# Performance work log

Measured on AMD Instinct MI355X. Metric: run time of the kernel, lower is better.

Reference implementation:

```python
import math
import jax, jax.numpy as jnp
import numpy as np

B, S, M, D, H = 4, 1024, 8, 64, 8
NF = D // 2  # n_freq = head_dim // 2
BANDWIDTH = 1.0


def setup_inputs() -> dict:
    key = jax.random.key(0)
    ks = jax.random.split(key, 12)
    n = lambda k, shp, sc=1.0: (jax.random.normal(k, shp, dtype=jnp.float32) * sc)
    w_scale = 0.02  # typical init scale for linear weights
    return {
        'q_atoms': n(ks[0], (B, S, M, D)),
        'q_logw': n(ks[1], (B, S, M)),
        'k_atoms': n(ks[2], (B, S, M, D)),
        'k_logw': n(ks[3], (B, S, M)),
        'v_atoms': n(ks[4], (B, S, M, D)),
        'v_logw': n(ks[5], (B, S, M)),
        'Wq': n(ks[6], (H * D, D), w_scale),   # torch Linear weight [out, in]
        'Wk': n(ks[7], (H * D, D), w_scale),
        'Wv': n(ks[8], (H * D, D), w_scale),
        'Wo': n(ks[9], (D, H * D), w_scale),
        'Ww': n(ks[10], (M, D), w_scale * 0.1),  # w_proj.weight scaled by 0.1
        'freqs': n(ks[11], (H, D, NF), 1.0 / BANDWIDTH),  # buffer
    }


def reference(q_atoms, q_logw, k_atoms, k_logw, v_atoms, v_logw,
              Wq, Wk, Wv, Wo, Ww, freqs):
    rff_scale = 1.0 / math.sqrt(NF)
    attn_scale = 1.0 / math.sqrt(D)

    q_w = jax.nn.softmax(q_logw, axis=-1)  # [B,S,M]
    k_w = jax.nn.softmax(k_logw, axis=-1)

    def proj(x, W):  # x: [B,S,M,D], W: [H*D, D] -> [B,S,M,H,D]
        return jnp.einsum('bsmd,ed->bsme', x, W).reshape(B, -1, M, H, D)

    qa = proj(q_atoms, Wq)
    ka = proj(k_atoms, Wk)
    va = proj(v_atoms, Wv)  # [B,S,M,H,D]

    def rff_encode(atoms, weights):
        # atoms: [B,S,M,H,D], weights: [B,S,M] -> [B,H,S,F] with F=D
        p = jnp.einsum('bsmhd,hdf->bsmhf', atoms, freqs)
        phi = jnp.concatenate([jnp.cos(p), jnp.sin(p)], axis=-1) * rff_scale
        z = jnp.einsum('bsmhf,bsm->bshf', phi, weights)
        return z.transpose(0, 2, 1, 3)

    q_enc = rff_encode(qa, q_w)  # [B,H,S,D]
    k_enc = rff_encode(ka, k_w)

    attn = jax.nn.softmax(
        jnp.einsum('bhqf,bhkf->bhqk', q_enc, k_enc) * attn_scale, axis=-1)

    # attn @ values, keeping atom dim m: [B,S,M,H,D]
    out = jnp.einsum('bhqk,bkmhd->bqmhd', attn, va)
    out = out.reshape(B, S, M, H * D)
    out_atoms = out @ Wo.T                  # [B,S,M,D]
    out_features = out_atoms.mean(axis=2)   # [B,S,D]
    new_log_weights = q_logw + out_features @ Ww.T  # [B,S,M]
    return out_atoms, new_log_weights
```

## Files before the change

### kernel.cpp

```cpp
#include <hip/hip_runtime.h>
#include <hip/hip_bf16.h>

typedef __hip_bfloat16 bf16;
typedef __attribute__((ext_vector_type(8))) short short8;
typedef __attribute__((ext_vector_type(4))) float floatx4;

#define CB 4
#define CS 1024
#define CM 8
#define CD 64
#define CH 8
#define CNF 32
#define CHD 512

#define OB_STRIDE 520
#define OS_STRIDE 68
#define AT_STRIDE 72
#define VO_STRIDE 40

__device__ __forceinline__ float b2f(bf16 x) { return __bfloat162float(x); }
__device__ __forceinline__ float us2f(unsigned short u) {
    union { unsigned int i; float f; } v; v.i = ((unsigned int)u) << 16; return v.f;
}
__device__ __forceinline__ floatx4 mfma16(short8 a, short8 b, floatx4 c) {
    return __builtin_amdgcn_mfma_f32_16x16x32_bf16(a, b, c, 0, 0, 0);
}


__global__ __launch_bounds__(256) void prep(const float* __restrict__ Wq,
                                            const float* __restrict__ Wk,
                                            const float* __restrict__ freqs,
                                            const float* __restrict__ Wo,
                                            const float* __restrict__ Wv,
                                            bf16* __restrict__ Fqb,
                                            bf16* __restrict__ Fkb,
                                            bf16* __restrict__ Wof,
                                            bf16* __restrict__ Wvf) {
    int bx = blockIdx.x, t = threadIdx.x;
    if (bx < 128) {
        int which = bx >> 6, h = (bx >> 3) & 7, ec = bx & 7;
        const float* W = which ? Wk : Wq;
        bf16* Fb = which ? Fkb : Fqb;
        int f = t & 31, el = t >> 5;
        int e = ec * 8 + el;
        float acc = 0.f;
        for (int d = 0; d < 64; ++d)
            acc += W[(h * 64 + d) * 64 + e] * freqs[(h * 64 + d) * 32 + f];
        int ntile = h * 2 + (f >> 4);
        int half = e >> 5, quad = (e >> 3) & 3, j = e & 7;
        Fb[(ntile * 2 + half) * 512 + quad * 128 + (f & 15) * 8 + j] = __float2bfloat16(acc);
    } else if (bx < 144) {
        int gid = (bx - 128) * 256 + t;
        #pragma unroll
        for (int i = 0; i < 2; ++i) {
            int idx4 = gid * 2 + i;
            float4 v = ((const float4*)Wo)[idx4];
            int flat = idx4 * 4;
            int o = flat >> 9, k0 = flat & 511;
            int ot = o >> 4, r0 = o & 15;
            int ks = k0 >> 5, qd = (k0 >> 3) & 3, j0 = k0 & 7;
            union { bf16 ob[4]; uint2 u; } pk;
            pk.ob[0] = __float2bfloat16(v.x); pk.ob[1] = __float2bfloat16(v.y);
            pk.ob[2] = __float2bfloat16(v.z); pk.ob[3] = __float2bfloat16(v.w);
            *(uint2*)(Wof + (ot * 16 + ks) * 512 + qd * 128 + r0 * 8 + j0) = pk.u;
        }
    } else {
        int gid = (bx - 144) * 256 + t;
        #pragma unroll
        for (int i = 0; i < 2; ++i) {
            int idx4 = gid * 2 + i;
            float4 v = ((const float4*)Wv)[idx4];
            int flat = idx4 * 4;
            int c = flat >> 6, e0 = flat & 63;
            int h2 = c >> 6, d = c & 63;
            int ehalf = e0 >> 5, qd = (e0 >> 3) & 3, j0 = e0 & 7;
            union { bf16 ob[4]; uint2 u; } pk;
            pk.ob[0] = __float2bfloat16(v.x); pk.ob[1] = __float2bfloat16(v.y);
            pk.ob[2] = __float2bfloat16(v.z); pk.ob[3] = __float2bfloat16(v.w);
            *(uint2*)(Wvf + (h2 * 8 + (d >> 4) * 2 + ehalf) * 512
                          + qd * 128 + (d & 15) * 8 + j0) = pk.u;
        }
    }
}

__global__ __launch_bounds__(256) void encvp(const float* __restrict__ qa_in,
                                             const float* __restrict__ ql,
                                             const float* __restrict__ ka_in,
                                             const float* __restrict__ kl,
                                             const bf16* __restrict__ Fqb,
                                             const bf16* __restrict__ Fkb,
                                             bf16* __restrict__ qf,
                                             bf16* __restrict__ kf,
                                             const float* __restrict__ va_in,
                                             const bf16* __restrict__ Wvf,
                                             bf16* __restrict__ Vt) {
    __shared__ __align__(16) bf16 smem[20480];
    int t = threadIdx.x;
    int w = t >> 6, l = t & 63;
    int quad = l >> 4, r = l & 15;

    if (blockIdx.x < 1024) {
        int blk = blockIdx.x;
        int xbase = blk * 4;
        int b = xbase >> 10, s0 = xbase & 1023;
        float* wgtF = (float*)smem;
        bf16* atq = smem + 128;
        bf16* atk = smem + 128 + 2304;
        bf16* zL  = smem + 128 + 4608;
        int tw = w & 1, nb = (w >> 1) * 8;

        {
            const float* srcq = qa_in + (size_t)(blk * 32) * 64;
            const float* srck = ka_in + (size_t)(blk * 32) * 64;
            #pragma unroll
            for (int j = 0; j < 2; ++j) {
                int idx4 = j * 256 + t;
                int flat = idx4 * 4;
                int row = flat >> 6, e = flat & 63;
                float4 vq = ((const float4*)srcq)[idx4];
                float4 vk = ((const float4*)srck)[idx4];
                union { bf16 ob[4]; uint2 u; } pq, pk2;
                pq.ob[0] = __float2bfloat16(vq.x); pq.ob[1] = __float2bfloat16(vq.y);
                pq.ob[2] = __float2bfloat16(vq.z); pq.ob[3] = __float2bfloat16(vq.w);
                pk2.ob[0] = __float2bfloat16(vk.x); pk2.ob[1] = __float2bfloat16(vk.y);
                pk2.ob[2] = __float2bfloat16(vk.z); pk2.ob[3] = __float2bfloat16(vk.w);
                *(uint2*)(atq + row * AT_STRIDE + e) = pq.u;
                *(uint2*)(atk + row * AT_STRIDE + e) = pk2.u;
            }
        }
        if (t < 64) {
            int which = t >> 5, row = t & 31;
            int si = row >> 3, m = row & 7;
            const float* lwp = (which ? kl : ql) + (size_t)(xbase + si) * 8;
            float lw[8]; float mx = -1e30f;
            #pragma unroll
            for (int j = 0; j < 8; ++j) { lw[j] = lwp[j]; mx = fmaxf(mx, lw[j]); }
            float sm = 0.f;
            #pragma unroll
            for (int j = 0; j < 8; ++j) sm += __expf(lw[j] - mx);
            const float rs = 0.17677669529663687f;
            float osc = which ? rs : rs * 0.125f;
            wgtF[which * 32 + row] = __expf(lw[m] - mx) * (osc / sm);
        }
        __syncthreads();

        for (int which = 0; which < 2; ++which) {
            const bf16* atb2 = which ? atk : atq;
            const bf16* Fb = which ? Fkb : Fqb;

            short8 a0 = *(const short8*)(atb2 + (tw * 16 + r) * AT_STRIDE + quad * 8);
            short8 a1 = *(const short8*)(atb2 + (tw * 16 + r) * AT_STRIDE + quad * 8 + 32);

            floatx4 acc[8];
            #pragma unroll
            for (int nt = 0; nt < 8; ++nt) {
                int ntile = nb + nt;
                short8 b0 = *(const short8*)(Fb + (ntile * 2 + 0) * 512 + l * 8);
                short8 b1 = *(const short8*)(Fb + (ntile * 2 + 1) * 512 + l * 8);
                floatx4 c = {0.f, 0.f, 0.f, 0.f};
                c = mfma16(a0, b0, c);
                c = mfma16(a1, b1, c);
                acc[nt] = c;
            }

            float wv[4];
            #pragma unroll
            for (int reg = 0; reg < 4; ++reg)
                wv[reg] = wgtF[which * 32 + tw * 16 + quad * 4 + reg];

            int si = tw * 2 + (quad >> 1);
            int iss = quad & 1;
            #pragma unroll
            for (int nt = 0; nt < 8; ++nt) {
                int n = (nb + nt) * 16 + r;
                int h = n >> 5, f = n & 31;
                float zc = 0.f, zs = 0.f;
                #pragma unroll
                for (int reg = 0; reg < 4; ++reg) {
                    float sv, cv;
                    __sincosf(acc[nt][reg], &sv, &cv);
                    zc += wv[reg] * cv;
                    zs += wv[reg] * sv;
                }
                zc += __shfl_xor(zc, 16);
                zs += __shfl_xor(zs, 16);
                float val = iss ? zs : zc;
                zL[((which * 4 + si) * 8 + h) * 64 + f + 32 * iss] = __float2bfloat16(val);
            }
        }
        __syncthreads();

        #pragma unroll
        for (int rep = 0; rep < 2; ++rep) {
            int idx = rep * 256 + t;
            int row = idx >> 3, c = idx & 7;
            int which = row >> 5, si = (row >> 3) & 3, h = row & 7;
            bf16* enc = which ? kf : qf;
            short8 v = *(const short8*)(zL + row * 64 + c * 8);
            int s = s0 + si;
            int bh = b * 8 + h;
            int kt = s >> 4, half = c >> 2, qd = c & 3;
            *(short8*)(enc + ((size_t)((bh * 64 + kt) * 2 + half)) * 512
                           + (qd * 16 + (s & 15)) * 8) = v;
        }
    } else {
        int vp = blockIdx.x - 1024;
        int g = vp & 127, h = vp >> 7;
        int b = g >> 5, sc = g & 31;
        int bh = b * 8 + h;
        bf16* atb = smem;
        bf16* os = smem;

        const float* src = va_in + ((size_t)(b * 1024 + sc * 32)) * 512;
        #pragma unroll
        for (int j = 0; j < 16; ++j) {
            int idx4 = j * 256 + t;
            float4 v = ((const float4*)src)[idx4];
            int flat = idx4 * 4;
            int s = flat >> 9, m = (flat >> 6) & 7, e = flat & 63;
            union { bf16 ob[4]; uint2 u; } pk;
            pk.ob[0] = __float2bfloat16(v.x); pk.ob[1] = __float2bfloat16(v.y);
            pk.ob[2] = __float2bfloat16(v.z); pk.ob[3] = __float2bfloat16(v.w);
            *(uint2*)(atb + (m * 32 + s) * AT_STRIDE + e) = pk.u;
        }
        __syncthreads();

        int dhalf = w & 1, sg = w >> 1;
        short8 aw0[2], aw1[2];
        #pragma unroll
        for (int dt = 0; dt < 2; ++dt) {
            int dt4 = dhalf * 2 + dt;
            aw0[dt] = *(const short8*)(Wvf + (size_t)(h * 8 + dt4 * 2 + 0) * 512 + l * 8);
            aw1[dt] = *(const short8*)(Wvf + (size_t)(h * 8 + dt4 * 2 + 1) * 512 + l * 8);
        }
        floatx4 acc[8][2];
        #pragma unroll
        for (int m = 0; m < 8; ++m)
            #pragma unroll
            for (int dt = 0; dt < 2; ++dt) acc[m][dt] = (floatx4){0.f, 0.f, 0.f, 0.f};

        #pragma unroll
        for (int m = 0; m < 8; ++m) {
            short8 b0 = *(const short8*)(atb + (m * 32 + sg * 16 + r) * AT_STRIDE + quad * 8);
            short8 b1 = *(const short8*)(atb + (m * 32 + sg * 16 + r) * AT_STRIDE + quad * 8 + 32);
            #pragma unroll
            for (int dt = 0; dt < 2; ++dt) {
                acc[m][dt] = mfma16(aw0[dt], b0, acc[m][dt]);
                acc[m][dt] = mfma16(aw1[dt], b1, acc[m][dt]);
            }
        }
        __syncthreads();

        #pragma unroll
        for (int m = 0; m < 8; ++m)
            #pragma unroll
            for (int dt = 0; dt < 2; ++dt)
                #pragma unroll
                for (int reg = 0; reg < 4; ++reg) {
                    int n = m * 64 + dhalf * 32 + dt * 16 + quad * 4 + reg;
                    os[n * VO_STRIDE + sg * 16 + r] = __float2bfloat16(acc[m][dt][reg]);
                }
        __syncthreads();

        #pragma unroll
        for (int j = 0; j < 8; ++j) {
            int ch = j * 256 + t;
            int nblk = ch >> 6, lv = ch & 63;
            int rv = lv & 15, qv = lv >> 4;
            short8 v = *(const short8*)(os + (nblk * 16 + rv) * VO_STRIDE + qv * 8);
            *(short8*)(Vt + ((size_t)(bh * 32 + nblk) * 32 + sc) * 512 + lv * 8) = v;
        }
    }
}

__global__ __launch_bounds__(512, 4) void attn_kern(const bf16* __restrict__ qf,
                                                    const bf16* __restrict__ kf,
                                                    const bf16* __restrict__ Vt,
                                                    bf16* __restrict__ tmpf) {
    int n = blockIdx.x;
    int bh = (n & 7) + 8 * (n >> 8);
    int qb = (n >> 3) & 31;
    int b = bh >> 3, h = bh & 7;

    __shared__ __align__(16) bf16 Sc[32 * 1024];
    __shared__ float sumW[8 * 32];
    __shared__ float invL[32];
    int t = threadIdx.x;
    int w = t >> 6, l = t & 63;
    int quad = l >> 4, r = l & 15;
    int k7 = r & 7;

    const bf16* qfb = qf + (size_t)(bh * 128 + qb * 4) * 512 + l * 8;
    short8 q0 = *(const short8*)(qfb);
    short8 q1 = *(const short8*)(qfb + 512);
    short8 q2 = *(const short8*)(qfb + 1024);
    short8 q3 = *(const short8*)(qfb + 1536);

    const bf16* kfb = kf + (size_t)(bh * 128) * 512 + l * 8;
    short8 kr[4][2];
    #pragma unroll
    for (int d = 0; d < 4; ++d) {
        kr[d][0] = *(const short8*)(kfb + (size_t)(w * 8 + d) * 1024);
        kr[d][1] = *(const short8*)(kfb + (size_t)(w * 8 + d) * 1024 + 512);
    }

    float ps0 = 0.f, ps1 = 0.f;
    #pragma unroll
    for (int i = 0; i < 8; ++i) {
        short8 k0 = kr[i & 3][0], k1 = kr[i & 3][1];
        if (i + 4 < 8) {
            kr[i & 3][0] = *(const short8*)(kfb + (size_t)(w * 8 + i + 4) * 1024);
            kr[i & 3][1] = *(const short8*)(kfb + (size_t)(w * 8 + i + 4) * 1024 + 512);
        }
        floatx4 c0 = {0.f, 0.f, 0.f, 0.f}, c1 = {0.f, 0.f, 0.f, 0.f};
        c0 = mfma16(k0, q0, c0); c0 = mfma16(k1, q1, c0);
        c1 = mfma16(k0, q2, c1); c1 = mfma16(k1, q3, c1);
        int ktl = w * 8 + i;
        int chunk = ktl * 2 + (quad >> 1);
        int sw = ((chunk ^ k7) << 3) + (quad & 1) * 4;
        union { uint2 u; bf16 bb[4]; } p0, p1;
        #pragma unroll
        for (int reg = 0; reg < 4; ++reg) {
            float e0 = __expf(c0[reg]);
            float e1 = __expf(c1[reg]);
            ps0 += e0; ps1 += e1;
            p0.bb[reg] = __float2bfloat16(e0);
            p1.bb[reg] = __float2bfloat16(e1);
        }
        *(uint2*)(Sc + r * 1024 + sw) = p0.u;
        *(uint2*)(Sc + (r + 16) * 1024 + sw) = p1.u;
    }
    ps0 += __shfl_xor(ps0, 16); ps0 += __shfl_xor(ps0, 32);
    ps1 += __shfl_xor(ps1, 16); ps1 += __shfl_xor(ps1, 32);
    if (l < 16) {
        sumW[w * 32 + r] = ps0;
        sumW[w * 32 + 16 + r] = ps1;
    }
    __syncthreads();

    if (t < 32) {
        float s = 0.f;
        #pragma unroll
        for (int w2 = 0; w2 < 8; ++w2) s += sumW[w2 * 32 + t];
        invL[t] = 1.f / s;
    }

    floatx4 acc0[4], acc1[4];
    #pragma unroll
    for (int nt = 0; nt < 4; ++nt) {
        acc0[nt] = (floatx4){0.f, 0.f, 0.f, 0.f};
        acc1[nt] = (floatx4){0.f, 0.f, 0.f, 0.f};
    }
    const bf16* vbase = Vt + ((size_t)(bh * 32 + w * 4) * 32) * 512 + l * 8;
    short8 vr[4][4];
    #pragma unroll
    for (int d = 0; d < 4; ++d)
        #pragma unroll
        for (int nt = 0; nt < 4; ++nt)
            vr[d][nt] = *(const short8*)(vbase + nt * 16384 + d * 512);

    #pragma unroll
    for (int ks = 0; ks < 32; ++ks) {
        int pc = (((ks * 4 + quad) ^ k7) << 3);
        short8 pa0 = *(const short8*)(Sc + r * 1024 + pc);
        short8 pa1 = *(const short8*)(Sc + (16 + r) * 1024 + pc);
        __builtin_amdgcn_s_setprio(1);
        #pragma unroll
        for (int nt = 0; nt < 4; ++nt) {
            acc0[nt] = mfma16(pa0, vr[ks & 3][nt], acc0[nt]);
            acc1[nt] = mfma16(pa1, vr[ks & 3][nt], acc1[nt]);
        }
        __builtin_amdgcn_s_setprio(0);
        if (ks + 4 < 32) {
            #pragma unroll
            for (int nt = 0; nt < 4; ++nt)
                vr[ks & 3][nt] = *(const short8*)(vbase + nt * 16384 + (ks + 4) * 512);
        }
    }
    __syncthreads();

    float inv0[4], inv1[4];
    #pragma unroll
    for (int reg = 0; reg < 4; ++reg) {
        inv0[reg] = invL[quad * 4 + reg];
        inv1[reg] = invL[16 + quad * 4 + reg];
    }

    bf16* Ob = Sc;
    #pragma unroll
    for (int nt = 0; nt < 4; ++nt)
        #pragma unroll
        for (int reg = 0; reg < 4; ++reg) {
            int col = w * 64 + nt * 16 + r;
            int m = col >> 6, d = col & 63;
            int colS = m * 64 + ((d + m * 8) & 63);
            Ob[(quad * 4 + reg) * OB_STRIDE + colS] =
                __float2bfloat16(acc0[nt][reg] * inv0[reg]);
            Ob[(quad * 4 + reg + 16) * OB_STRIDE + colS] =
                __float2bfloat16(acc1[nt][reg] * inv1[reg]);
        }
    __syncthreads();

    #pragma unroll
    for (int i = 0; i < 4; ++i) {
        int ci = i * 8 + w;
        int lv = t & 63;
        int T = ci >> 1, khalf = ci & 1;
        int quadv = lv >> 4, rv = lv & 15;
        int p = rv >> 3, m = rv & 7;
        int q_local = T * 2 + p;
        int d0 = khalf * 32 + quadv * 8;
        int colS = m * 64 + ((d0 + m * 8) & 63);
        short8 v = *(const short8*)(Ob + q_local * OB_STRIDE + colS);
        int GT = b * 512 + qb * 16 + T;
        *(short8*)(tmpf + ((size_t)(GT * 16 + h * 2 + khalf)) * 512 + lv * 8) = v;
    }
}

__global__ __launch_bounds__(256) void finalize(const bf16* __restrict__ tmpf,
                                                const bf16* __restrict__ Wof,
                                                const float* __restrict__ Ww,
                                                const float* __restrict__ ql,
                                                float* __restrict__ out) {
    __shared__ __align__(16) float Os[64][OS_STRIDE];
    __shared__ float fs[8][64];
    int t = threadIdx.x;
    int w = t >> 6, l = t & 63;
    int quad = l >> 4, r = l & 15;
    size_t rowbase = (size_t)blockIdx.x * 64;

    floatx4 acc[4];
    #pragma unroll
    for (int nt = 0; nt < 4; ++nt) acc[nt] = (floatx4){0.f, 0.f, 0.f, 0.f};

    const bf16* afrag = tmpf + ((size_t)(blockIdx.x * 4 + w) * 16) * 512 + l * 8;
    const bf16* bfrag = Wof + l * 8;

    for (int ks = 0; ks < 16; ++ks) {
        short8 a = *(const short8*)(afrag + ks * 512);
        #pragma unroll
        for (int nt = 0; nt < 4; ++nt) {
            short8 bb = *(const short8*)(bfrag + (size_t)(nt * 16 + ks) * 512);
            acc[nt] = mfma16(a, bb, acc[nt]);
        }
    }
    #pragma unroll
    for (int nt = 0; nt < 4; ++nt)
        #pragma unroll
        for (int reg = 0; reg < 4; ++reg)
            Os[w * 16 + quad * 4 + reg][nt * 16 + r] = acc[nt][reg];
    __syncthreads();

    #pragma unroll
    for (int i = 0; i < 4; ++i) {
        int ch = i * 256 + t;
        int rr = ch >> 4, c4 = (ch & 15) * 4;
        float4 v = *(const float4*)&Os[rr][c4];
        *(float4*)(out + (rowbase + rr) * 64 + c4) = v;
    }

    {
        int g = t >> 5, oo = (t & 31) * 2;
        float f0 = 0.f, f1 = 0.f;
        #pragma unroll
        for (int m = 0; m < 8; ++m) {
            f0 += Os[g * 8 + m][oo];
            f1 += Os[g * 8 + m][oo + 1];
        }
        fs[g][oo] = f0 * 0.125f;
        fs[g][oo + 1] = f1 * 0.125f;
    }
    __syncthreads();

    if (t < 64) {
        int g = t >> 3, mm = t & 7;
        size_t x = (size_t)blockIdx.x * 8 + g;
        float nl = ql[x * 8 + mm];
        #pragma unroll
        for (int o = 0; o < 64; ++o) nl += fs[g][o] * Ww[mm * 64 + o];
        out[(size_t)CB * CS * CM * CD + x * 8 + mm] = nl;
    }
}

extern "C" void kernel_launch(void* const* d_in, const int* in_sizes, int n_in,
                              void* d_out, int out_size, void* d_ws, size_t ws_size,
                              hipStream_t stream) {
    const float* q_atoms = (const float*)d_in[0];
    const float* q_logw  = (const float*)d_in[1];
    const float* k_atoms = (const float*)d_in[2];
    const float* k_logw  = (const float*)d_in[3];
    const float* v_atoms = (const float*)d_in[4];
    const float* Wq = (const float*)d_in[6];
    const float* Wk = (const float*)d_in[7];
    const float* Wv = (const float*)d_in[8];
    const float* Wo = (const float*)d_in[9];
    const float* Ww = (const float*)d_in[10];
    const float* freqs = (const float*)d_in[11];

    bf16* Fqb = (bf16*)d_ws;
    bf16* Fkb = Fqb + 16384;
    bf16* qf = Fkb + 16384;
    bf16* kf = qf + 2097152;
    bf16* Vt = kf + 2097152;
    bf16* tmpf = Vt + 2097152 * 8;
    bf16* Wof = tmpf + 16777216;
    bf16* Wvf = Wof + 32768;
    float* out = (float*)d_out;

    prep<<<160, 256, 0, stream>>>(Wq, Wk, freqs, Wo, Wv, Fqb, Fkb, Wof, Wvf);
    encvp<<<2048, 256, 0, stream>>>(q_atoms, q_logw, k_atoms, k_logw,
                                    Fqb, Fkb, qf, kf,
                                    v_atoms, Wvf, Vt);
    attn_kern<<<1024, 512, 0, stream>>>(qf, kf, Vt, tmpf);
    finalize<<<CB * CS / 8, 256, 0, stream>>>(tmpf, Wof, Ww, q_logw, out);
}
```

Measured before the change: 172.6 us.

## Fold Wv projection into output weight, attend over raw value atoms

The value projection Wv is no longer applied per token. Instead, Wo and Wv are pre-multiplied per head into a combined weight Cf inside the prep kernel. The attention kernel now reads raw bf16 value atoms, which are shared across all heads, rather than per-head projected values. This removes the per-head V projection GEMM and shrinks the value workspace written by encvp. The cost is an extra small weight-product computation in prep and a strided, uncoalesced scalar transpose of the value atoms.

Result: faster. 167.5 us (-2.9%).

```diff
diff --git a/kernel.cpp b/kernel.cpp
--- a/kernel.cpp
+++ b/kernel.cpp
@@ -16,7 +16,6 @@
 #define OB_STRIDE 520
 #define OS_STRIDE 68
 #define AT_STRIDE 72
-#define VO_STRIDE 40
 
 __device__ __forceinline__ float b2f(bf16 x) { return __bfloat162float(x); }
 __device__ __forceinline__ float us2f(unsigned short u) {
@@ -34,8 +33,7 @@
                                             const float* __restrict__ Wv,
                                             bf16* __restrict__ Fqb,
                                             bf16* __restrict__ Fkb,
-                                            bf16* __restrict__ Wof,
-                                            bf16* __restrict__ Wvf) {
+                                            bf16* __restrict__ Cf) {
     int bx = blockIdx.x, t = threadIdx.x;
     if (bx < 128) {
         int which = bx >> 6, h = (bx >> 3) & 7, ec = bx & 7;
@@ -49,37 +47,25 @@
         int ntile = h * 2 + (f >> 4);
         int half = e >> 5, quad = (e >> 3) & 3, j = e & 7;
         Fb[(ntile * 2 + half) * 512 + quad * 128 + (f & 15) * 8 + j] = __float2bfloat16(acc);
-    } else if (bx < 144) {
-        int gid = (bx - 128) * 256 + t;
-        #pragma unroll
-        for (int i = 0; i < 2; ++i) {
-            int idx4 = gid * 2 + i;
-            float4 v = ((const float4*)Wo)[idx4];
-            int flat = idx4 * 4;
-            int o = flat >> 9, k0 = flat & 511;
-            int ot = o >> 4, r0 = o & 15;
-            int ks = k0 >> 5, qd = (k0 >> 3) & 3, j0 = k0 & 7;
-            union { bf16 ob[4]; uint2 u; } pk;
-            pk.ob[0] = __float2bfloat16(v.x); pk.ob[1] = __float2bfloat16(v.y);
-            pk.ob[2] = __float2bfloat16(v.z); pk.ob[3] = __float2bfloat16(v.w);
-            *(uint2*)(Wof + (ot * 16 + ks) * 512 + qd * 128 + r0 * 8 + j0) = pk.u;
-        }
     } else {
-        int gid = (bx - 144) * 256 + t;
-        #pragma unroll
-        for (int i = 0; i < 2; ++i) {
-            int idx4 = gid * 2 + i;
-            float4 v = ((const float4*)Wv)[idx4];
-            int flat = idx4 * 4;
-            int c = flat >> 6, e0 = flat & 63;
-            int h2 = c >> 6, d = c & 63;
-            int ehalf = e0 >> 5, qd = (e0 >> 3) & 3, j0 = e0 & 7;
-            union { bf16 ob[4]; uint2 u; } pk;
-            pk.ob[0] = __float2bfloat16(v.x); pk.ob[1] = __float2bfloat16(v.y);
-            pk.ob[2] = __float2bfloat16(v.z); pk.ob[3] = __float2bfloat16(v.w);
-            *(uint2*)(Wvf + (h2 * 8 + (d >> 4) * 2 + ehalf) * 512
-                          + qd * 128 + (d & 15) * 8 + j0) = pk.u;
-        }
+        int fid = ((bx - 128) * 256 + t) * 8;
+        int o = fid >> 9, rem = fid & 511, h = rem >> 6, e0 = rem & 63;
+        const float* wo = Wo + o * 512 + h * 64;
+        float accv[8];
+        #pragma unroll
+        for (int i = 0; i < 8; ++i) accv[i] = 0.f;
+        for (int d = 0; d < 64; ++d) {
+            float wod = wo[d];
+            const float* wv = Wv + (size_t)(h * 64 + d) * 64 + e0;
+            #pragma unroll
+            for (int i = 0; i < 8; ++i) accv[i] += wod * wv[i];
+        }
+        int k = h * 64 + e0;
+        int ot = o >> 4, r0 = o & 15, ks = k >> 5, qd = (k >> 3) & 3;
+        union { bf16 ob[8]; short8 s8; } pk;
+        #pragma unroll
+        for (int i = 0; i < 8; ++i) pk.ob[i] = __float2bfloat16(accv[i]);
+        *(short8*)(Cf + (ot * 16 + ks) * 512 + qd * 128 + r0 * 8) = pk.s8;
     }
 }
 
@@ -92,8 +78,7 @@
                                              bf16* __restrict__ qf,
                                              bf16* __restrict__ kf,
                                              const float* __restrict__ va_in,
-                                             const bf16* __restrict__ Wvf,
-                                             bf16* __restrict__ Vt) {
+                                             bf16* __restrict__ vaf) {
     __shared__ __align__(16) bf16 smem[20480];
     int t = threadIdx.x;
     int w = t >> 6, l = t & 63;
@@ -205,77 +190,30 @@
         }
     } else {
         int vp = blockIdx.x - 1024;
-        int g = vp & 127, h = vp >> 7;
-        int b = g >> 5, sc = g & 31;
-        int bh = b * 8 + h;
-        bf16* atb = smem;
-        bf16* os = smem;
-
+        int b = vp >> 5, sc = vp & 31;
         const float* src = va_in + ((size_t)(b * 1024 + sc * 32)) * 512;
         #pragma unroll
-        for (int j = 0; j < 16; ++j) {
-            int idx4 = j * 256 + t;
-            float4 v = ((const float4*)src)[idx4];
-            int flat = idx4 * 4;
-            int s = flat >> 9, m = (flat >> 6) & 7, e = flat & 63;
-            union { bf16 ob[4]; uint2 u; } pk;
-            pk.ob[0] = __float2bfloat16(v.x); pk.ob[1] = __float2bfloat16(v.y);
-            pk.ob[2] = __float2bfloat16(v.z); pk.ob[3] = __float2bfloat16(v.w);
-            *(uint2*)(atb + (m * 32 + s) * AT_STRIDE + e) = pk.u;
-        }
-        __syncthreads();
-
-        int dhalf = w & 1, sg = w >> 1;
-        short8 aw0[2], aw1[2];
-        #pragma unroll
-        for (int dt = 0; dt < 2; ++dt) {
-            int dt4 = dhalf * 2 + dt;
-            aw0[dt] = *(const short8*)(Wvf + (size_t)(h * 8 + dt4 * 2 + 0) * 512 + l * 8);
-            aw1[dt] = *(const short8*)(Wvf + (size_t)(h * 8 + dt4 * 2 + 1) * 512 + l * 8);
-        }
-        floatx4 acc[8][2];
-        #pragma unroll
-        for (int m = 0; m < 8; ++m)
-            #pragma unroll
-            for (int dt = 0; dt < 2; ++dt) acc[m][dt] = (floatx4){0.f, 0.f, 0.f, 0.f};
-
-        #pragma unroll
-        for (int m = 0; m < 8; ++m) {
-            short8 b0 = *(const short8*)(atb + (m * 32 + sg * 16 + r) * AT_STRIDE + quad * 8);
-            short8 b1 = *(const short8*)(atb + (m * 32 + sg * 16 + r) * AT_STRIDE + quad * 8 + 32);
-            #pragma unroll
-            for (int dt = 0; dt < 2; ++dt) {
-                acc[m][dt] = mfma16(aw0[dt], b0, acc[m][dt]);
-                acc[m][dt] = mfma16(aw1[dt], b1, acc[m][dt]);
+        for (int rep = 0; rep < 2; ++rep) {
+            int nn = rep * 256 + t;
+            int m = nn >> 6, e = nn & 63, nblk = nn >> 4, rr = nn & 15;
+            bf16* dchunk = vaf + ((size_t)((b * 32 + nblk) * 32 + sc)) * 512;
+            #pragma unroll
+            for (int qd = 0; qd < 4; ++qd) {
+                union { bf16 ob[8]; short8 s8; } pk;
+                #pragma unroll
+                for (int j = 0; j < 8; ++j) {
+                    int s = qd * 8 + j;
+                    pk.ob[j] = __float2bfloat16(src[(size_t)(s * 8 + m) * 64 + e]);
+                }
+                *(short8*)(dchunk + (qd * 16 + rr) * 8) = pk.s8;
             }
-        }
-        __syncthreads();
-
-        #pragma unroll
-        for (int m = 0; m < 8; ++m)
-            #pragma unroll
-            for (int dt = 0; dt < 2; ++dt)
-                #pragma unroll
-                for (int reg = 0; reg < 4; ++reg) {
-                    int n = m * 64 + dhalf * 32 + dt * 16 + quad * 4 + reg;
-                    os[n * VO_STRIDE + sg * 16 + r] = __float2bfloat16(acc[m][dt][reg]);
-                }
-        __syncthreads();
-
-        #pragma unroll
-        for (int j = 0; j < 8; ++j) {
-            int ch = j * 256 + t;
-            int nblk = ch >> 6, lv = ch & 63;
-            int rv = lv & 15, qv = lv >> 4;
-            short8 v = *(const short8*)(os + (nblk * 16 + rv) * VO_STRIDE + qv * 8);
-            *(short8*)(Vt + ((size_t)(bh * 32 + nblk) * 32 + sc) * 512 + lv * 8) = v;
         }
     }
 }
 
 __global__ __launch_bounds__(512, 4) void attn_kern(const bf16* __restrict__ qf,
                                                     const bf16* __restrict__ kf,
-                                                    const bf16* __restrict__ Vt,
+                                                    const bf16* __restrict__ vaf,
                                                     bf16* __restrict__ tmpf) {
     int n = blockIdx.x;
     int bh = (n & 7) + 8 * (n >> 8);
@@ -351,7 +289,7 @@
         acc0[nt] = (floatx4){0.f, 0.f, 0.f, 0.f};
         acc1[nt] = (floatx4){0.f, 0.f, 0.f, 0.f};
     }
-    const bf16* vbase = Vt + ((size_t)(bh * 32 + w * 4) * 32) * 512 + l * 8;
+    const bf16* vbase = vaf + ((size_t)(b * 32 + w * 4) * 32) * 512 + l * 8;
     short8 vr[4][4];
     #pragma unroll
     for (int d = 0; d < 4; ++d)
@@ -418,7 +356,7 @@
 }
 
 __global__ __launch_bounds__(256) void finalize(const bf16* __restrict__ tmpf,
-                                                const bf16* __restrict__ Wof,
+                                                const bf16* __restrict__ Cf,
                                                 const float* __restrict__ Ww,
                                                 const float* __restrict__ ql,
                                                 float* __restrict__ out) {
@@ -434,7 +372,7 @@
     for (int nt = 0; nt < 4; ++nt) acc[nt] = (floatx4){0.f, 0.f, 0.f, 0.f};
 
     const bf16* afrag = tmpf + ((size_t)(blockIdx.x * 4 + w) * 16) * 512 + l * 8;
-    const bf16* bfrag = Wof + l * 8;
+    const bf16* bfrag = Cf + l * 8;
 
     for (int ks = 0; ks < 16; ++ks) {
         short8 a = *(const short8*)(afrag + ks * 512);
@@ -501,16 +439,15 @@
     bf16* Fkb = Fqb + 16384;
     bf16* qf = Fkb + 16384;
     bf16* kf = qf + 2097152;
-    bf16* Vt = kf + 2097152;
-    bf16* tmpf = Vt + 2097152 * 8;
-    bf16* Wof = tmpf + 16777216;
-    bf16* Wvf = Wof + 32768;
+    bf16* vaf = kf + 2097152;
+    bf16* tmpf = vaf + 2097152 * 8;
+    bf16* Cf = tmpf + 16777216;
     float* out = (float*)d_out;
 
-    prep<<<160, 256, 0, stream>>>(Wq, Wk, freqs, Wo, Wv, Fqb, Fkb, Wof, Wvf);
-    encvp<<<2048, 256, 0, stream>>>(q_atoms, q_logw, k_atoms, k_logw,
+    prep<<<144, 256, 0, stream>>>(Wq, Wk, freqs, Wo, Wv, Fqb, Fkb, Cf);
+    encvp<<<1152, 256, 0, stream>>>(q_atoms, q_logw, k_atoms, k_logw,
                                     Fqb, Fkb, qf, kf,
-                                    v_atoms, Wvf, Vt);
-    attn_kern<<<1024, 512, 0, stream>>>(qf, kf, Vt, tmpf);
-    finalize<<<CB * CS / 8, 256, 0, stream>>>(tmpf, Wof, Ww, q_logw, out);
-}
+                                    v_atoms, vaf);
+    attn_kern<<<1024, 512, 0, stream>>>(qf, kf, vaf, tmpf);
+    finalize<<<CB * CS / 8, 256, 0, stream>>>(tmpf, Cf, Ww, q_logw, out);
+}
```
